# Performance work log

Hardware: AMD Instinct MI355X
Metric: run time of the kernel (lower is better)

The kernel has to match this reference:

```python
import jax, jax.numpy as jnp
import numpy as np

SEQ = 8192
EMB = 1024
MID = 1024


def setup_inputs() -> dict:
    key = jax.random.key(0)
    ks = jax.random.split(key, 7)
    s = 1.0 / np.sqrt(EMB)
    return {
        "text_encoded": jax.random.normal(ks[0], (SEQ, EMB), dtype=jnp.float32),
        "Wq": jax.random.normal(ks[1], (MID, EMB), dtype=jnp.float32) * s,
        "bq": jax.random.normal(ks[2], (MID,), dtype=jnp.float32) * 0.02,
        "Wk": jax.random.normal(ks[3], (MID, EMB), dtype=jnp.float32) * s,
        "bk": jax.random.normal(ks[4], (MID,), dtype=jnp.float32) * 0.02,
        "Wv": jax.random.normal(ks[5], (MID, EMB), dtype=jnp.float32) * s,
        "bv": jax.random.normal(ks[6], (MID,), dtype=jnp.float32) * 0.02,
    }


def reference(text_encoded, Wq, bq, Wk, bk, Wv, bv):
    # torch nn.Linear: y = x @ W.T + b, W is [out, in]
    Q = text_encoded @ Wq.T + bq  # [S, M]
    K = text_encoded @ Wk.T + bk  # [S, M]
    V = text_encoded @ Wv.T + bv  # [S, M]
    # cosine-similarity scores: (Q K^T) scaled by outer(1/||Q||, 1/||K||)
    inv_qn = jax.lax.rsqrt(jnp.sum(Q * Q, axis=1))  # [S]
    inv_kn = jax.lax.rsqrt(jnp.sum(K * K, axis=1))  # [S]
    scores = (Q @ K.T) * (inv_qn[:, None] * inv_kn[None, :])  # [S, S]
    weights = jax.nn.softmax(scores, axis=1)
    return weights @ V  # [S, M]
```

## Files before the change

### kernel.cpp

```cpp
#include <hip/hip_runtime.h>


#define SEQ 8192
#define MID 1024
#define EMB 1024

typedef __attribute__((ext_vector_type(8))) short short8x;
typedef __attribute__((ext_vector_type(16))) float float16x;
typedef __attribute__((ext_vector_type(4))) int int4x;
typedef __attribute__((ext_vector_type(16))) int int16x;

__device__ __forceinline__ unsigned short f2bf(float x) {
  union { float f; unsigned u; } v; v.f = x;
  unsigned r = v.u + 0x7FFFu + ((v.u >> 16) & 1u);
  return (unsigned short)(r >> 16);
}
__device__ __forceinline__ float bf2f(unsigned short h) {
  union { unsigned u; float f; } v; v.u = ((unsigned)h) << 16;
  return v.f;
}
__device__ __forceinline__ float fexp2(float x) {
#if __has_builtin(__builtin_amdgcn_exp2f)
  return __builtin_amdgcn_exp2f(x);
#else
  return __expf(x * 0.6931471805599453f);
#endif
}

__device__ __forceinline__ void g2l16(const void* g, void* lds) {
  __builtin_amdgcn_global_load_lds(
      (const __attribute__((address_space(1))) unsigned int*)g,
      (__attribute__((address_space(3))) unsigned int*)lds, 16, 0, 0);
}

__device__ __forceinline__ void gemm128_nt(
    const unsigned short* __restrict__ A, const unsigned short* __restrict__ B,
    long lda, long ldb, int m0, int n0, int K,
    unsigned short* As, unsigned short* Bs, float16x acc[2][2]) {
  const int tid = threadIdx.x;
  const int w = tid >> 6;
  const int l = tid & 63;
  const int wm = (w & 1) << 6;
  const int wn = (w >> 1) << 6;
  const int srow = l >> 3;
  const int skg = (l & 7) ^ srow;
  const int l31 = l & 31;
  const int lh = l >> 5;
  const int swz = l31 & 7;

  for (int k0 = 0; k0 < K; k0 += 64) {
    __syncthreads();
#pragma unroll
    for (int r = 0; r < 4; ++r) {
      const int rr = (w * 4 + r) * 8 + srow;
      g2l16(A + (long)(m0 + rr) * lda + k0 + skg * 8, As + (w * 4 + r) * 512);
      g2l16(B + (long)(n0 + rr) * ldb + k0 + skg * 8, Bs + (w * 4 + r) * 512);
    }
    __syncthreads();
#pragma unroll
    for (int ks = 0; ks < 4; ++ks) {
      const int kg = ks * 2 + lh;
      short8x av[2], bv[2];
#pragma unroll
      for (int t = 0; t < 2; ++t) {
        av[t] = *(const short8x*)(As + (wm + t * 32 + l31) * 64 + ((kg ^ swz) << 3));
        bv[t] = *(const short8x*)(Bs + (wn + t * 32 + l31) * 64 + ((kg ^ swz) << 3));
      }
#pragma unroll
      for (int tm = 0; tm < 2; ++tm)
#pragma unroll
        for (int tn = 0; tn < 2; ++tn)
          acc[tm][tn] = __builtin_amdgcn_mfma_f32_32x32x16_bf16(av[tm], bv[tn], acc[tm][tn], 0, 0, 0);
    }
  }
}

__device__ __forceinline__ void gemm128_nt_i8(
    const unsigned char* __restrict__ A, const unsigned char* __restrict__ B,
    long lda, long ldb, int m0, int n0, int Kbytes,
    unsigned char* As, unsigned char* Bs, int16x acc[2][2]) {
  const int tid = threadIdx.x;
  const int w = tid >> 6;
  const int l = tid & 63;
  const int wm = (w & 1) << 6;
  const int wn = (w >> 1) << 6;
  const int srow = l >> 3;
  const int skg = (l & 7) ^ srow;
  const int l31 = l & 31;
  const int lh = l >> 5;
  const int swz = l31 & 7;

  for (int k0 = 0; k0 < Kbytes; k0 += 128) {
    __syncthreads();
#pragma unroll
    for (int r = 0; r < 4; ++r) {
      const int rr = (w * 4 + r) * 8 + srow;
      g2l16(A + (long)(m0 + rr) * lda + k0 + skg * 16, As + (w * 4 + r) * 1024);
      g2l16(B + (long)(n0 + rr) * ldb + k0 + skg * 16, Bs + (w * 4 + r) * 1024);
    }
    __syncthreads();
#pragma unroll
    for (int ks = 0; ks < 4; ++ks) {
      const int kg = ks * 2 + lh;
      int4x av[2], bv[2];
#pragma unroll
      for (int t = 0; t < 2; ++t) {
        av[t] = *(const int4x*)(As + (wm + t * 32 + l31) * 128 + ((kg ^ swz) << 4));
        bv[t] = *(const int4x*)(Bs + (wn + t * 32 + l31) * 128 + ((kg ^ swz) << 4));
      }
#pragma unroll
      for (int tm = 0; tm < 2; ++tm)
#pragma unroll
        for (int tn = 0; tn < 2; ++tn)
          acc[tm][tn] = __builtin_amdgcn_mfma_i32_32x32x32_i8(av[tm], bv[tn], acc[tm][tn], 0, 0, 0);
    }
  }
}

__device__ __forceinline__ void gemm256x128_nt_i8(
    const unsigned char* __restrict__ A, const unsigned char* __restrict__ B,
    long lda, long ldb, int m0, int n0, int Kbytes,
    unsigned char* As, unsigned char* Bs, int16x acc[4][2]) {
  const int tid = threadIdx.x;
  const int w = tid >> 6;
  const int l = tid & 63;
  const int wm = (w & 1) << 7;
  const int wn = (w >> 1) << 6;
  const int srow = l >> 3;
  const int skg = (l & 7) ^ srow;
  const int l31 = l & 31;
  const int lh = l >> 5;
  const int swz = l31 & 7;

  for (int k0 = 0; k0 < Kbytes; k0 += 128) {
    __syncthreads();
#pragma unroll
    for (int r = 0; r < 8; ++r) {
      const int rr = (w * 8 + r) * 8 + srow;
      g2l16(A + (long)(m0 + rr) * lda + k0 + skg * 16, As + (w * 8 + r) * 1024);
    }
#pragma unroll
    for (int r = 0; r < 4; ++r) {
      const int rr = (w * 4 + r) * 8 + srow;
      g2l16(B + (long)(n0 + rr) * ldb + k0 + skg * 16, Bs + (w * 4 + r) * 1024);
    }
    __syncthreads();
#pragma unroll
    for (int ks = 0; ks < 4; ++ks) {
      const int kg = ks * 2 + lh;
      int4x av[4], bv[2];
#pragma unroll
      for (int t = 0; t < 4; ++t)
        av[t] = *(const int4x*)(As + (wm + t * 32 + l31) * 128 + ((kg ^ swz) << 4));
#pragma unroll
      for (int t = 0; t < 2; ++t)
        bv[t] = *(const int4x*)(Bs + (wn + t * 32 + l31) * 128 + ((kg ^ swz) << 4));
#pragma unroll
      for (int tm = 0; tm < 4; ++tm)
#pragma unroll
        for (int tn = 0; tn < 2; ++tn)
          acc[tm][tn] = __builtin_amdgcn_mfma_i32_32x32x32_i8(av[tm], bv[tn], acc[tm][tn], 0, 0, 0);
    }
  }
}

__global__ void cvt_all(const float* __restrict__ X,
                        const float* __restrict__ wq, const float* __restrict__ wk,
                        const float* __restrict__ wv,
                        unsigned short* __restrict__ Xb, unsigned short* __restrict__ Wb,
                        float* __restrict__ sums) {
  const long i = ((long)blockIdx.x * 256 + threadIdx.x) * 4;
  if (i < 24576) *(float4*)(sums + i) = (float4){0.f, 0.f, 0.f, 0.f};
  const float* src;
  unsigned short* dst;
  long off;
  if (i < (long)SEQ * EMB) {
    src = X; dst = Xb; off = i;
  } else {
    long j = i - (long)SEQ * EMB;
    int t = (int)(j >> 20);
    off = j & (MID * EMB - 1);
    src = (t == 0) ? wq : (t == 1) ? wk : wv;
    dst = Wb + (long)t * MID * EMB;
  }
  float4 v = *(const float4*)(src + off);
  ushort4 o;
  o.x = f2bf(v.x); o.y = f2bf(v.y); o.z = f2bf(v.z); o.w = f2bf(v.w);
  *(ushort4*)(dst + off) = o;
}

__global__ __launch_bounds__(256) void qkv_kernel(
    const unsigned short* __restrict__ Xb, const unsigned short* __restrict__ Wb,
    const float* __restrict__ bq, const float* __restrict__ bk, const float* __restrict__ bv,
    unsigned char* __restrict__ Q8, unsigned char* __restrict__ K8,
    unsigned char* __restrict__ VT8, float* __restrict__ sumsq) {
  __shared__ unsigned short smem[16384];
  unsigned short* As = smem;
  unsigned short* Bs = smem + 8192;
  const int z = blockIdx.z;
  const int m0 = blockIdx.y * 128;
  const int n0 = blockIdx.x * 128;
  float16x acc[2][2];
#pragma unroll
  for (int i = 0; i < 2; ++i)
#pragma unroll
    for (int j = 0; j < 2; ++j)
#pragma unroll
      for (int e = 0; e < 16; ++e) acc[i][j][e] = 0.f;

  gemm128_nt(Xb, Wb + (long)z * MID * EMB, EMB, EMB, m0, n0, EMB, As, Bs, acc);

  const int tid = threadIdx.x;
  const int l = tid & 63, w = tid >> 6;
  const int wm = (w & 1) << 6, wn = (w >> 1) << 6;
  const int l31 = l & 31, lh = l >> 5;
  const float* bias = (z == 0) ? bq : (z == 1) ? bk : bv;
  float bvv[2];
#pragma unroll
  for (int tn = 0; tn < 2; ++tn) bvv[tn] = bias[n0 + wn + tn * 32 + l31];
#pragma unroll
  for (int tm = 0; tm < 2; ++tm)
#pragma unroll
    for (int tn = 0; tn < 2; ++tn)
#pragma unroll
      for (int r = 0; r < 16; ++r) acc[tm][tn][r] += bvv[tn];

  __syncthreads();

  if (z < 2) {
#pragma unroll
    for (int tm = 0; tm < 2; ++tm)
#pragma unroll
      for (int tn = 0; tn < 2; ++tn) {
        const int rcol = wn + tn * 32 + l31;
#pragma unroll
        for (int r = 0; r < 16; ++r) {
          float v = acc[tm][tn][r];
          float po = __shfl_xor(v, 1);
          if (!(l & 1)) {
            const int rrow = wm + tm * 32 + (r & 3) + 8 * (r >> 2) + 4 * lh;
            const int chunk = (rcol >> 3) ^ (rrow & 7);
            unsigned pk = (unsigned)f2bf(v) | ((unsigned)f2bf(po) << 16);
            *(unsigned*)(smem + rrow * 128 + (chunk << 3) + (rcol & 7)) = pk;
          }
        }
      }
    __syncthreads();
    unsigned char* O8 = z ? K8 : Q8;
    float* ss = sumsq + (long)z * SEQ;
    const float qs = 127.0f / 8.0f;
#pragma unroll
    for (int round = 0; round < 8; ++round) {
      const int row = round * 16 + (tid >> 4);
      const int c = tid & 15;
      short8x vv = *(const short8x*)(smem + row * 128 + ((c ^ (row & 7)) << 3));
      int qq[8];
      float s = 0.f;
#pragma unroll
      for (int j = 0; j < 8; ++j) {
        float t = rintf(bf2f((unsigned short)vv[j]) * qs);
        t = fminf(127.f, fmaxf(-127.f, t));
        qq[j] = (int)t;
        s += t * t;
      }
      unsigned lo = (qq[0] & 255) | ((qq[1] & 255) << 8) | ((qq[2] & 255) << 16) | ((qq[3] & 255) << 24);
      unsigned hi = (qq[4] & 255) | ((qq[5] & 255) << 8) | ((qq[6] & 255) << 16) | ((qq[7] & 255) << 24);
      int2 pk; pk.x = (int)lo; pk.y = (int)hi;
      *(int2*)(O8 + (long)(m0 + row) * MID + n0 + c * 8) = pk;
      s += __shfl_xor(s, 1); s += __shfl_xor(s, 2);
      s += __shfl_xor(s, 4); s += __shfl_xor(s, 8);
      if (c == 0) atomicAdd(ss + m0 + row, s);
    }
  } else {
#pragma unroll
    for (int tm = 0; tm < 2; ++tm)
#pragma unroll
      for (int tn = 0; tn < 2; ++tn) {
        const int nn = wn + tn * 32 + l31;
#pragma unroll
        for (int g = 0; g < 4; ++g) {
          const int mm = wm + tm * 32 + 8 * g + 4 * lh;
          const int chunk = (mm >> 3) ^ (nn & 7);
          ushort4 pk;
          pk.x = f2bf(acc[tm][tn][g * 4 + 0]);
          pk.y = f2bf(acc[tm][tn][g * 4 + 1]);
          pk.z = f2bf(acc[tm][tn][g * 4 + 2]);
          pk.w = f2bf(acc[tm][tn][g * 4 + 3]);
          *(ushort4*)(smem + nn * 128 + (chunk << 3) + (mm & 7)) = pk;
        }
      }
    __syncthreads();
    const float vs = 127.0f / 6.0f;
#pragma unroll
    for (int round = 0; round < 8; ++round) {
      const int nn = round * 16 + (tid >> 4);
      const int c = tid & 15;
      short8x vv = *(const short8x*)(smem + nn * 128 + ((c ^ (nn & 7)) << 3));
      int qq[8];
#pragma unroll
      for (int j = 0; j < 8; ++j) {
        float t = rintf(bf2f((unsigned short)vv[j]) * vs);
        t = fminf(127.f, fmaxf(-127.f, t));
        qq[j] = (int)t;
      }
      unsigned lo = (qq[0] & 255) | ((qq[1] & 255) << 8) | ((qq[2] & 255) << 16) | ((qq[3] & 255) << 24);
      unsigned hi = (qq[4] & 255) | ((qq[5] & 255) << 8) | ((qq[6] & 255) << 16) | ((qq[7] & 255) << 24);
      int2 pk; pk.x = (int)lo; pk.y = (int)hi;
      *(int2*)(VT8 + (long)(n0 + nn) * SEQ + m0 + c * 8) = pk;
    }
  }
}

__global__ __launch_bounds__(256, 2) void score_kernel(
    const unsigned char* __restrict__ Q8, const unsigned char* __restrict__ K8,
    const float* __restrict__ sumsq,
    unsigned char* __restrict__ P8, float* __restrict__ denomq) {
  __shared__ unsigned char smem8[49152];
  unsigned char* As = smem8;
  unsigned char* Bs = smem8 + 32768;
  const int kb0 = blockIdx.x * 256;
  const int qb0 = blockIdx.y * 128;
  int16x acc[4][2];
#pragma unroll
  for (int i = 0; i < 4; ++i)
#pragma unroll
    for (int j = 0; j < 2; ++j)
#pragma unroll
      for (int e = 0; e < 16; ++e) acc[i][j][e] = 0;

  gemm256x128_nt_i8(K8, Q8, MID, MID, kb0, qb0, MID, As, Bs, acc);

  const int tid = threadIdx.x;
  const int l = tid & 63, w = tid >> 6;
  const int wm = (w & 1) << 7, wn = (w >> 1) << 6;
  const int l31 = l & 31, lh = l >> 5;

  const float LOG2E  = 1.4426950408889634f;
  const float LOG2PS = 5.5459896458832860f;
  const float MAGIC  = 12582912.0f;
  float qi[2];
#pragma unroll
  for (int tn = 0; tn < 2; ++tn)
    qi[tn] = rsqrtf(sumsq[qb0 + wn + tn * 32 + l31]) * LOG2E;

  __syncthreads();

  unsigned char* Plds = As;
#pragma unroll
  for (int tm = 0; tm < 4; ++tm) {
#pragma unroll
    for (int g = 0; g < 4; ++g) {
      const int nb = wm + tm * 32 + g * 8 + lh * 4;
      float4 ss4 = *(const float4*)(sumsq + SEQ + kb0 + nb);
      float ik0 = rsqrtf(ss4.x), ik1 = rsqrtf(ss4.y);
      float ik2 = rsqrtf(ss4.z), ik3 = rsqrtf(ss4.w);
#pragma unroll
      for (int tn = 0; tn < 2; ++tn) {
        unsigned u0 = __float_as_uint(fexp2(fmaf((float)acc[tm][tn][g * 4 + 0] * ik0, qi[tn], LOG2PS)) + MAGIC);
        unsigned u1 = __float_as_uint(fexp2(fmaf((float)acc[tm][tn][g * 4 + 1] * ik1, qi[tn], LOG2PS)) + MAGIC);
        unsigned u2 = __float_as_uint(fexp2(fmaf((float)acc[tm][tn][g * 4 + 2] * ik2, qi[tn], LOG2PS)) + MAGIC);
        unsigned u3 = __float_as_uint(fexp2(fmaf((float)acc[tm][tn][g * 4 + 3] * ik3, qi[tn], LOG2PS)) + MAGIC);
        unsigned pk = (u0 & 255) | ((u1 & 255) << 8) | ((u2 & 255) << 16) | (u3 << 24);
        const int ml = wn + tn * 32 + l31;
        const int addr = ml * 256 + ((((nb >> 4) ^ (ml & 15)) << 4) | (nb & 15));
        *(unsigned*)(Plds + addr) = pk;
      }
    }
  }
  __syncthreads();

  const unsigned M8 = 0x00FF00FFu;
#pragma unroll
  for (int round = 0; round < 8; ++round) {
    const int row = round * 16 + (tid >> 4);
    const int c = tid & 15;
    const int addr = row * 256 + ((c ^ (row & 15)) << 4);
    uint4 v = *(const uint4*)(Plds + addr);
    unsigned e = (v.x & M8) + (v.y & M8) + (v.z & M8) + (v.w & M8);
    unsigned o = ((v.x >> 8) & M8) + ((v.y >> 8) & M8) + ((v.z >> 8) & M8) + ((v.w >> 8) & M8);
    unsigned t = e + o;
    unsigned s = (t & 0xFFFFu) + (t >> 16);
    *(uint4*)(P8 + (long)(qb0 + row) * SEQ + kb0 + c * 16) = v;
    s += __shfl_xor(s, 1); s += __shfl_xor(s, 2);
    s += __shfl_xor(s, 4); s += __shfl_xor(s, 8);
    if (c == 0) atomicAdd(denomq + qb0 + row, (float)s);
  }
}

__global__ __launch_bounds__(256, 4) void out_kernel(
    const unsigned char* __restrict__ P8, const unsigned char* __restrict__ VT8,
    const float* __restrict__ denomq, float* __restrict__ out) {
  __shared__ unsigned char smem8[32768];
  unsigned char* As = smem8;
  unsigned char* Bs = smem8 + 16384;
  const int n0 = blockIdx.x * 128;
  const int m0 = blockIdx.y * 128;
  int16x acc[2][2];
#pragma unroll
  for (int i = 0; i < 2; ++i)
#pragma unroll
    for (int j = 0; j < 2; ++j)
#pragma unroll
      for (int e = 0; e < 16; ++e) acc[i][j][e] = 0;

  gemm128_nt_i8(P8, VT8, SEQ, SEQ, m0, n0, SEQ, As, Bs, acc);

  const int l = threadIdx.x & 63, w = threadIdx.x >> 6;
  const int wm = (w & 1) << 6, wn = (w >> 1) << 6;
  const int l31 = l & 31, lh = l >> 5;
  const float sv = 127.0f / 6.0f;
#pragma unroll
  for (int tm = 0; tm < 2; ++tm)
#pragma unroll
    for (int r = 0; r < 16; ++r) {
      const int row = m0 + wm + tm * 32 + (r & 3) + 8 * (r >> 2) + 4 * lh;
      const float inv = 1.0f / (sv * denomq[row]);
#pragma unroll
      for (int tn = 0; tn < 2; ++tn) {
        const int col = n0 + wn + tn * 32 + l31;
        out[(long)row * MID + col] = (float)acc[tm][tn][r] * inv;
      }
    }
}

extern "C" void kernel_launch(void* const* d_in, const int* in_sizes, int n_in,
                              void* d_out, int out_size, void* d_ws, size_t ws_size,
                              hipStream_t stream) {
  const float* X  = (const float*)d_in[0];
  const float* Wq = (const float*)d_in[1];
  const float* bq = (const float*)d_in[2];
  const float* Wk = (const float*)d_in[3];
  const float* bk = (const float*)d_in[4];
  const float* Wv = (const float*)d_in[5];
  const float* bv = (const float*)d_in[6];

  char* wsb = (char*)d_ws;
  const size_t MB = 1ull << 20;
  unsigned char* Q8  = (unsigned char*)(wsb);
  unsigned char* K8  = (unsigned char*)(wsb + 8 * MB);
  unsigned char* VT8 = (unsigned char*)(wsb + 16 * MB);
  float* sums        = (float*)(wsb + 24 * MB);
  float* denomq      = sums + 2 * SEQ;
  unsigned char* P8  = (unsigned char*)(wsb + 25 * MB);
  unsigned short* Xb = (unsigned short*)(wsb + 25 * MB);
  unsigned short* Wb = (unsigned short*)(wsb + 41 * MB);

  const int cvt_elems = SEQ * EMB + 3 * MID * EMB;
  cvt_all<<<cvt_elems / 1024, 256, 0, stream>>>(X, Wq, Wk, Wv, Xb, Wb, sums);

  qkv_kernel<<<dim3(MID / 128, SEQ / 128, 3), 256, 0, stream>>>(Xb, Wb, bq, bk, bv, Q8, K8, VT8, sums);
  score_kernel<<<dim3(SEQ / 256, SEQ / 128), 256, 0, stream>>>(Q8, K8, sums, P8, denomq);
  out_kernel<<<dim3(MID / 128, SEQ / 128), 256, 0, stream>>>(P8, VT8, denomq, (float*)d_out);
}
```

Measured before the change: 354.0 us.

## Double-buffer score GEMM with 512-thread 256x256 tiles and ping-pong scheduling

Replaces the single-buffered 256x128 int8 score GEMM with a 512-thread block that computes a 256x256 tile. K and Q slices are double-buffered in 128 KB of LDS, and the next k-slice is prefetched while MFMAs run, with s_setprio and barrier interleaving between waves. This aims to hide global-load latency and raise reuse per block. The cost is lower occupancy (one block per CU given LDS use) and more barriers per iteration.

```diff
diff --git a/kernel.cpp b/kernel.cpp
--- a/kernel.cpp
+++ b/kernel.cpp
@@ -110,53 +110,6 @@
       }
 #pragma unroll
       for (int tm = 0; tm < 2; ++tm)
-#pragma unroll
-        for (int tn = 0; tn < 2; ++tn)
-          acc[tm][tn] = __builtin_amdgcn_mfma_i32_32x32x32_i8(av[tm], bv[tn], acc[tm][tn], 0, 0, 0);
-    }
-  }
-}
-
-__device__ __forceinline__ void gemm256x128_nt_i8(
-    const unsigned char* __restrict__ A, const unsigned char* __restrict__ B,
-    long lda, long ldb, int m0, int n0, int Kbytes,
-    unsigned char* As, unsigned char* Bs, int16x acc[4][2]) {
-  const int tid = threadIdx.x;
-  const int w = tid >> 6;
-  const int l = tid & 63;
-  const int wm = (w & 1) << 7;
-  const int wn = (w >> 1) << 6;
-  const int srow = l >> 3;
-  const int skg = (l & 7) ^ srow;
-  const int l31 = l & 31;
-  const int lh = l >> 5;
-  const int swz = l31 & 7;
-
-  for (int k0 = 0; k0 < Kbytes; k0 += 128) {
-    __syncthreads();
-#pragma unroll
-    for (int r = 0; r < 8; ++r) {
-      const int rr = (w * 8 + r) * 8 + srow;
-      g2l16(A + (long)(m0 + rr) * lda + k0 + skg * 16, As + (w * 8 + r) * 1024);
-    }
-#pragma unroll
-    for (int r = 0; r < 4; ++r) {
-      const int rr = (w * 4 + r) * 8 + srow;
-      g2l16(B + (long)(n0 + rr) * ldb + k0 + skg * 16, Bs + (w * 4 + r) * 1024);
-    }
-    __syncthreads();
-#pragma unroll
-    for (int ks = 0; ks < 4; ++ks) {
-      const int kg = ks * 2 + lh;
-      int4x av[4], bv[2];
-#pragma unroll
-      for (int t = 0; t < 4; ++t)
-        av[t] = *(const int4x*)(As + (wm + t * 32 + l31) * 128 + ((kg ^ swz) << 4));
-#pragma unroll
-      for (int t = 0; t < 2; ++t)
-        bv[t] = *(const int4x*)(Bs + (wn + t * 32 + l31) * 128 + ((kg ^ swz) << 4));
-#pragma unroll
-      for (int tm = 0; tm < 4; ++tm)
 #pragma unroll
         for (int tn = 0; tn < 2; ++tn)
           acc[tm][tn] = __builtin_amdgcn_mfma_i32_32x32x32_i8(av[tm], bv[tn], acc[tm][tn], 0, 0, 0);
@@ -311,15 +264,24 @@
   }
 }
 
-__global__ __launch_bounds__(256, 2) void score_kernel(
+__global__ __launch_bounds__(512) void score_kernel(
     const unsigned char* __restrict__ Q8, const unsigned char* __restrict__ K8,
     const float* __restrict__ sumsq,
     unsigned char* __restrict__ P8, float* __restrict__ denomq) {
-  __shared__ unsigned char smem8[49152];
-  unsigned char* As = smem8;
-  unsigned char* Bs = smem8 + 32768;
+  __shared__ unsigned char smem8[131072];
+  const int tid = threadIdx.x;
+  const int w = tid >> 6;
+  const int l = tid & 63;
+  const int wm = (w & 1) << 7;
+  const int wn = (w >> 1) << 6;
+  const int srow = l >> 3;
+  const int skg = (l & 7) ^ srow;
+  const int l31 = l & 31;
+  const int lh = l >> 5;
+  const int swz = l31 & 7;
   const int kb0 = blockIdx.x * 256;
-  const int qb0 = blockIdx.y * 128;
+  const int qb0 = blockIdx.y * 256;
+
   int16x acc[4][2];
 #pragma unroll
   for (int i = 0; i < 4; ++i)
@@ -328,12 +290,54 @@
 #pragma unroll
       for (int e = 0; e < 16; ++e) acc[i][j][e] = 0;
 
-  gemm256x128_nt_i8(K8, Q8, MID, MID, kb0, qb0, MID, As, Bs, acc);
-
-  const int tid = threadIdx.x;
-  const int l = tid & 63, w = tid >> 6;
-  const int wm = (w & 1) << 7, wn = (w >> 1) << 6;
-  const int l31 = l & 31, lh = l >> 5;
+#define SCORE_STAGE(kt_) do {                                                        \
+    unsigned char* As_ = smem8 + (((kt_) & 1) << 16);                                \
+    unsigned char* Bs_ = As_ + 32768;                                                \
+    const int k0_ = (kt_) * 128;                                                     \
+    _Pragma("unroll")                                                                \
+    for (int r = 0; r < 4; ++r) {                                                    \
+      const int rr = (w * 4 + r) * 8 + srow;                                         \
+      g2l16(K8 + (long)(kb0 + rr) * MID + k0_ + skg * 16, As_ + (w * 4 + r) * 1024); \
+      g2l16(Q8 + (long)(qb0 + rr) * MID + k0_ + skg * 16, Bs_ + (w * 4 + r) * 1024); \
+    }                                                                                \
+  } while (0)
+
+  SCORE_STAGE(0);
+  asm volatile("s_waitcnt vmcnt(0)" ::: "memory");
+  __builtin_amdgcn_s_barrier();
+
+#pragma unroll 1
+  for (int kt = 0; kt < 8; ++kt) {
+    unsigned char* As = smem8 + ((kt & 1) << 16);
+    unsigned char* Bs = As + 32768;
+    int4x bv[2][4];
+#pragma unroll
+    for (int tn = 0; tn < 2; ++tn)
+#pragma unroll
+      for (int ks = 0; ks < 4; ++ks)
+        bv[tn][ks] = *(const int4x*)(Bs + (wn + tn * 32 + l31) * 128 + (((ks * 2 + lh) ^ swz) << 4));
+#pragma unroll
+    for (int tm = 0; tm < 4; ++tm) {
+      int4x av[4];
+#pragma unroll
+      for (int ks = 0; ks < 4; ++ks)
+        av[ks] = *(const int4x*)(As + (wm + tm * 32 + l31) * 128 + (((ks * 2 + lh) ^ swz) << 4));
+      if (tm == 0 && kt < 7) SCORE_STAGE(kt + 1);
+      __builtin_amdgcn_s_barrier();
+      __builtin_amdgcn_s_setprio(1);
+#pragma unroll
+      for (int ks = 0; ks < 4; ++ks)
+#pragma unroll
+        for (int tn = 0; tn < 2; ++tn)
+          acc[tm][tn] = __builtin_amdgcn_mfma_i32_32x32x32_i8(av[ks], bv[tn][ks], acc[tm][tn], 0, 0, 0);
+      __builtin_amdgcn_s_setprio(0);
+      if (tm == 3) asm volatile("s_waitcnt vmcnt(0)" ::: "memory");
+      __builtin_amdgcn_s_barrier();
+    }
+  }
+#undef SCORE_STAGE
+
+  __syncthreads();
 
   const float LOG2E  = 1.4426950408889634f;
   const float LOG2PS = 5.5459896458832860f;
@@ -343,9 +347,7 @@
   for (int tn = 0; tn < 2; ++tn)
     qi[tn] = rsqrtf(sumsq[qb0 + wn + tn * 32 + l31]) * LOG2E;
 
-  __syncthreads();
-
-  unsigned char* Plds = As;
+  unsigned char* Plds = smem8;
 #pragma unroll
   for (int tm = 0; tm < 4; ++tm) {
 #pragma unroll
@@ -372,7 +374,7 @@
   const unsigned M8 = 0x00FF00FFu;
 #pragma unroll
   for (int round = 0; round < 8; ++round) {
-    const int row = round * 16 + (tid >> 4);
+    const int row = round * 32 + (tid >> 4);
     const int c = tid & 15;
     const int addr = row * 256 + ((c ^ (row & 15)) << 4);
     uint4 v = *(const uint4*)(Plds + addr);
@@ -449,6 +451,6 @@
   cvt_all<<<cvt_elems / 1024, 256, 0, stream>>>(X, Wq, Wk, Wv, Xb, Wb, sums);
 
   qkv_kernel<<<dim3(MID / 128, SEQ / 128, 3), 256, 0, stream>>>(Xb, Wb, bq, bk, bv, Q8, K8, VT8, sums);
-  score_kernel<<<dim3(SEQ / 256, SEQ / 128), 256, 0, stream>>>(Q8, K8, sums, P8, denomq);
+  score_kernel<<<dim3(SEQ / 256, SEQ / 256), 512, 0, stream>>>(Q8, K8, sums, P8, denomq);
   out_kernel<<<dim3(MID / 128, SEQ / 128), 256, 0, stream>>>(P8, VT8, denomq, (float*)d_out);
 }
```

Result: faster. 340.9 us (-3.7%).
